# Performance work log

Hardware: AMD Instinct MI355X
Metric: run time of the kernel (lower is better)

The kernel has to match this reference:

```python
import jax, jax.numpy as jnp
import numpy as np

B, T, DIM, HEADS, DH, MLP = 2, 1024, 768, 8, 96, 3072
EPS = 1e-6


def _rms_norm(x, w):
    return x * jax.lax.rsqrt(jnp.mean(x * x, axis=-1, keepdims=True) + EPS) * w


def _rotate_half(x):
    x1, x2 = jnp.split(x, 2, axis=-1)
    return jnp.concatenate([-x2, x1], axis=-1)


def _l2norm(x):
    n = jnp.sqrt(jnp.sum(x * x, axis=-1, keepdims=True))
    return x / jnp.maximum(n, 1e-12)


def setup_inputs() -> dict:
    key = jax.random.key(0)
    ks = jax.random.split(key, 16)
    def rn(k, shape, s=0.02):
        return jax.random.normal(k, shape, jnp.float32) * s
    return {
        'x_stream1': jax.random.normal(ks[0], (B, T, DIM), jnp.float32),
        'x_stream2': jax.random.normal(ks[1], (B, T, DIM), jnp.float32),
        'p_emb': jax.random.normal(ks[2], (B, 1, 1024), jnp.float32),
        'mod_w1': rn(ks[3], (1024, 512)), 'mod_b1': jnp.zeros((512,), jnp.float32),
        'mod_w2': rn(ks[4], (512, DIM * 12)), 'mod_b2': jnp.zeros((DIM * 12,), jnp.float32),
        'norm11_w': jnp.ones((DIM,), jnp.float32), 'norm12_w': jnp.ones((DIM,), jnp.float32),
        'qkv_w': rn(ks[5], (DIM, 3 * DIM)), 'qkv_b': jnp.zeros((3 * DIM,), jnp.float32),
        'qkv2_w': rn(ks[6], (DIM, 3 * DIM)), 'qkv2_b': jnp.zeros((3 * DIM,), jnp.float32),
        'qk_scale': jnp.full((DH,), 10.0, jnp.float32),
        'out_w': rn(ks[7], (DIM, DIM)), 'out_b': jnp.zeros((DIM,), jnp.float32),
        'norm21_w': jnp.ones((DIM,), jnp.float32), 'norm22_w': jnp.ones((DIM,), jnp.float32),
        'mlp1_w1': rn(ks[8], (DIM, MLP)), 'mlp1_b1': jnp.zeros((MLP,), jnp.float32),
        'mlp1_w2': rn(ks[9], (MLP, DIM)), 'mlp1_b2': jnp.zeros((DIM,), jnp.float32),
        'mlp2_w1': rn(ks[10], (DIM, MLP)), 'mlp2_b1': jnp.zeros((MLP,), jnp.float32),
        'mlp2_w2': rn(ks[11], (MLP, DIM)), 'mlp2_b2': jnp.zeros((DIM,), jnp.float32),
    }


def _forward(x_stream1, x_stream2, p_emb, mod_w1, mod_b1, mod_w2, mod_b2,
             norm11_w, norm12_w, qkv_w, qkv_b, qkv2_w, qkv2_b, qk_scale,
             out_w, out_b, norm21_w, norm22_w,
             mlp1_w1, mlp1_b1, mlp1_w2, mlp1_b2,
             mlp2_w1, mlp2_b1, mlp2_w2, mlp2_b2):
    Bc, Tc, D = x_stream1.shape
    # modulation MLP: SiLU -> Linear -> SiLU -> Linear -> 12 chunks of [B, D]
    h = jax.nn.silu(p_emb[:, 0, :])
    h = jax.nn.silu(h @ mod_w1 + mod_b1)
    mod = h @ mod_w2 + mod_b2
    (m1s, m1h, m1g, m2s, m2h, m2g,
     m3s, m3h, m3g, m4s, m4h, m4g) = [m[:, None, :] for m in jnp.split(mod, 12, axis=1)]

    xm1 = _rms_norm(x_stream1, norm11_w) * (1 + m1s) + m1h
    xm2 = _rms_norm(x_stream2, norm12_w) * (1 + m2s) + m2h

    q1, k1, v1 = jnp.split(xm1 @ qkv_w + qkv_b, 3, axis=-1)
    q2, k2, v2 = jnp.split(xm2 @ qkv2_w + qkv2_b, 3, axis=-1)
    q = jnp.concatenate([q1, q2], axis=1)  # [B, 2T, D]
    k = jnp.concatenate([k1, k2], axis=1)
    v = jnp.concatenate([v1, v2], axis=1)
    N = 2 * Tc

    def to_heads(x):
        return x.reshape(Bc, N, HEADS, DH).transpose(0, 2, 1, 3)  # [B, H, N, dh]
    q, k, v = to_heads(q), to_heads(k), to_heads(v)

    # RoPE (inv_freq computed in bf16 as in the original, then used in fp32)
    inv_freq = (1.0 / (10000.0 ** (jnp.arange(0, DH, 2, dtype=jnp.float32) / DH))).astype(jnp.bfloat16).astype(jnp.float32)
    t = jnp.arange(N, dtype=jnp.float32)
    freqs = t[:, None] * inv_freq[None, :]
    emb = jnp.concatenate([freqs, freqs], axis=-1)  # [N, dh]
    cos, sin = jnp.cos(emb), jnp.sin(emb)
    q = q * cos + _rotate_half(q) * sin
    k = k * cos + _rotate_half(k) * sin

    # QK-Norm
    q = _l2norm(q) * qk_scale
    k = _l2norm(k) * qk_scale

    scores = jnp.einsum('bhid,bhjd->bhij', q, k) * (DH ** -0.5)
    probs = jax.nn.softmax(scores, axis=-1)
    attn = jnp.einsum('bhij,bhjd->bhid', probs, v)
    attn = attn.transpose(0, 2, 1, 3).reshape(Bc, N, D)
    attn = attn @ out_w + out_b

    x1 = x_stream1 + attn[:, :Tc, :] * m1g
    x2 = x_stream2 + attn[:, Tc:, :] * m2g

    xn1 = _rms_norm(x1, norm21_w) * (1 + m3s) + m3h
    mlp1 = jax.nn.gelu(xn1 @ mlp1_w1 + mlp1_b1, approximate=False) @ mlp1_w2 + mlp1_b2
    xn2 = _rms_norm(x2, norm22_w) * (1 + m4s) + m4h
    mlp2 = jax.nn.gelu(xn2 @ mlp2_w1 + mlp2_b1, approximate=False) @ mlp2_w2 + mlp2_b2

    return (x1 + mlp1 * m3g, x2 + mlp2 * m4g)


def reference(x_stream1, x_stream2, p_emb, mod_w1, mod_b1, mod_w2, mod_b2,
              norm11_w, norm12_w, qkv_w, qkv_b, qkv2_w, qkv2_b, qk_scale,
              out_w, out_b, norm21_w, norm22_w,
              mlp1_w1, mlp1_b1, mlp1_w2, mlp1_b2,
              mlp2_w1, mlp2_b1, mlp2_w2, mlp2_b2):
    return _forward(x_stream1, x_stream2, p_emb, mod_w1, mod_b1, mod_w2, mod_b2,
                    norm11_w, norm12_w, qkv_w, qkv_b, qkv2_w, qkv2_b, qk_scale,
                    out_w, out_b, norm21_w, norm22_w,
                    mlp1_w1, mlp1_b1, mlp1_w2, mlp1_b2,
                    mlp2_w1, mlp2_b1, mlp2_w2, mlp2_b2)
```

## Files before the change

kernel.cpp:

```cpp
#include <hip/hip_runtime.h>
#include <hip/hip_bf16.h>
#include <cstdint>
#include <math.h>

#define BB 2
#define TT 1024
#define DIMM 768
#define NHEADS 8
#define DHH 96
#define MLPD 3072
#define NN 2048

typedef unsigned short u16;
using short8 = __attribute__((ext_vector_type(8))) short;
using f32x4  = __attribute__((ext_vector_type(4))) float;
using f32x16 = __attribute__((ext_vector_type(16))) float;
using int4v  = __attribute__((ext_vector_type(4))) int;
union S8I4 { int4v i; short8 s; };

static constexpr float kEps = 1e-6f;

__device__ __forceinline__ float siluf(float x){ return x / (1.f + expf(-x)); }
__device__ __forceinline__ float geluf(float x){ return 0.5f*x*(1.f + erff(x*0.7071067811865475f)); }
__device__ __forceinline__ float bf16_rne(float x){
  uint32_t u = __float_as_uint(x);
  u = (u + 0x7fffu + ((u >> 16) & 1u)) & 0xffff0000u;
  return __uint_as_float(u);
}
__device__ __forceinline__ u16 f2b(float x){
  uint32_t u = __float_as_uint(x);
  return (u16)((u + 0x7fffu + ((u >> 16) & 1u)) >> 16);
}
__device__ __forceinline__ float b2f(u16 b){
  return __uint_as_float(((uint32_t)b) << 16);
}
__device__ __forceinline__ int cvtpk(float lo, float hi){
  int d; asm("v_cvt_pk_bf16_f32 %0, %1, %2" : "=v"(d) : "v"(lo), "v"(hi)); return d;
}
__device__ __forceinline__ void gload16(const void* g, void* l){
  __builtin_amdgcn_global_load_lds((const __attribute__((address_space(1))) unsigned int*)g,
                                   (__attribute__((address_space(3))) unsigned int*)l, 16, 0, 0);
}

__global__ __launch_bounds__(256) void mod_stage1_k(
    const float* __restrict__ p_emb, const float* __restrict__ w1,
    const float* __restrict__ b1, float* __restrict__ h2){
  __shared__ float sp[1024];
  const int b = blockIdx.x >> 1;
  const int obase = (blockIdx.x & 1) * 256;
  for (int i = threadIdx.x; i < 1024; i += 256)
    sp[i] = siluf(p_emb[b*1024 + i]);
  __syncthreads();
  const int o = obase + threadIdx.x;
  float acc = 0.f;
  for (int j = 0; j < 1024; ++j) acc += sp[j] * w1[j*512 + o];
  h2[b*512 + o] = siluf(acc + b1[o]);
}

__global__ __launch_bounds__(256) void mod_stage2_k(
    const float* __restrict__ h2, const float* __restrict__ w2,
    const float* __restrict__ b2, float* __restrict__ mod){
  __shared__ float sh[512];
  const int b = blockIdx.x / 36;
  const int obase = (blockIdx.x % 36) * 256;
  for (int i = threadIdx.x; i < 512; i += 256)
    sh[i] = h2[b*512 + i];
  __syncthreads();
  const int o = obase + threadIdx.x;
  float acc = 0.f;
  for (int j = 0; j < 512; ++j) acc += sh[j] * w2[j*9216 + o];
  mod[b*9216 + o] = acc + b2[o];
}

__global__ __launch_bounds__(256) void wt_all_k(
    const float* __restrict__ s0, u16* __restrict__ d0,
    const float* __restrict__ s1, u16* __restrict__ d1,
    const float* __restrict__ s2, u16* __restrict__ d2,
    const float* __restrict__ s3, u16* __restrict__ d3,
    const float* __restrict__ s4, u16* __restrict__ d4,
    const float* __restrict__ s5, u16* __restrict__ d5,
    const float* __restrict__ s6, u16* __restrict__ d6){
  const int bid = blockIdx.x;
  const float* S; u16* D; int K, N, lid;
  if      (bid < 432)  { S=s0; D=d0; K=768;  N=2304; lid=bid; }
  else if (bid < 864)  { S=s1; D=d1; K=768;  N=2304; lid=bid-432; }
  else if (bid < 1008) { S=s2; D=d2; K=768;  N=768;  lid=bid-864; }
  else if (bid < 1584) { S=s3; D=d3; K=768;  N=3072; lid=bid-1008; }
  else if (bid < 2160) { S=s4; D=d4; K=3072; N=768;  lid=bid-1584; }
  else if (bid < 2736) { S=s5; D=d5; K=768;  N=3072; lid=bid-2160; }
  else                 { S=s6; D=d6; K=3072; N=768;  lid=bid-2736; }
  const int nx = N >> 6;
  const int k0 = (lid / nx) * 64, n0 = (lid % nx) * 64;
  __shared__ float t[64][65];
  const int tx = threadIdx.x & 63, ty = threadIdx.x >> 6;
  for (int i = ty; i < 64; i += 4)
    t[i][tx] = S[(size_t)(k0+i)*N + n0 + tx];
  __syncthreads();
  for (int i = ty; i < 64; i += 4)
    D[(size_t)(n0+i)*K + k0 + tx] = f2b(t[tx][i]);
}

__global__ __launch_bounds__(256) void rmsnorm2_k(
    const float* __restrict__ x0, const float* __restrict__ w0, int cs0, int ch0, u16* __restrict__ o0,
    const float* __restrict__ x1, const float* __restrict__ w1, int cs1, int ch1, u16* __restrict__ o1,
    const float* __restrict__ mod){
  const int rowg = blockIdx.x;
  const int s = rowg >> 11;
  const int row = rowg & 2047;
  const float* x = s ? x1 : x0;
  const float* w = s ? w1 : w0;
  const int cs = s ? cs1 : cs0, ch = s ? ch1 : ch0;
  u16* out = s ? o1 : o0;
  const int b = row >> 10;
  const int tid = threadIdx.x;
  const float* xr = x + (size_t)row * DIMM;
  float v0 = xr[tid], v1 = xr[tid + 256], v2 = xr[tid + 512];
  float ss = v0*v0 + v1*v1 + v2*v2;
  __shared__ float red[4];
  for (int m = 1; m < 64; m <<= 1) ss += __shfl_xor(ss, m, 64);
  if ((tid & 63) == 0) red[tid >> 6] = ss;
  __syncthreads();
  float tot = red[0] + red[1] + red[2] + red[3];
  float rms = rsqrtf(tot * (1.f/768.f) + kEps);
  const float* ms = mod + (size_t)b*9216 + (size_t)cs*768;
  const float* mh = mod + (size_t)b*9216 + (size_t)ch*768;
  u16* orow = out + (size_t)row * DIMM;
  orow[tid]       = f2b(v0*rms*w[tid]      *(1.f+ms[tid])       + mh[tid]);
  orow[tid + 256] = f2b(v1*rms*w[tid+256]  *(1.f+ms[tid+256])   + mh[tid+256]);
  orow[tid + 512] = f2b(v2*rms*w[tid+512]  *(1.f+ms[tid+512])   + mh[tid+512]);
}

template<int EPI, int DUAL>
__global__ __launch_bounds__(256, 6) void gemm64_k(
    const u16* __restrict__ A0, const u16* __restrict__ Bt0,
    const float* __restrict__ bias0, void* __restrict__ C0,
    const u16* __restrict__ A1, const u16* __restrict__ Bt1,
    const float* __restrict__ bias1, void* __restrict__ C1,
    int M, int N, int K){
  __shared__ u16 As[2][64*32];
  __shared__ u16 Bs[2][64*32];
  const int z = DUAL ? blockIdx.z : 0;
  const u16* A      = z ? A1 : A0;
  const u16* Bt     = z ? Bt1 : Bt0;
  const float* bias = z ? bias1 : bias0;
  void* C           = z ? C1 : C0;
  const int tid = threadIdx.x;
  const int w = tid >> 6, l = tid & 63;
  const int wr = w >> 1, wc = w & 1;
  const int la = l & 15, hi4 = l >> 4;
  const int m0 = blockIdx.y*64, n0 = blockIdx.x*64;
  f32x4 acc[2][2] = {};
  const int nk = K >> 5;
  const int srow = tid >> 2;
  const int scol = ((tid & 3) ^ ((srow >> 1) & 3)) * 8;
  const u16* Ap = A  + (size_t)(m0 + srow)*K + scol;
  const u16* Bp = Bt + (size_t)(n0 + srow)*K + scol;
  #define STAGE(buf, kofs) { \
    gload16(Ap + (kofs), &As[buf][tid*8]); \
    gload16(Bp + (kofs), &Bs[buf][tid*8]); }
  STAGE(0, 0);
  __syncthreads();
  const int rslot = (hi4 ^ ((l >> 1) & 3)) * 8;
  for (int kt = 0; kt < nk; ++kt){
    const int cur = kt & 1;
    if (kt + 1 < nk) STAGE(cur^1, (kt+1) << 5);
    short8 af[2], bf[2];
    #pragma unroll
    for (int mi = 0; mi < 2; ++mi)
      af[mi] = *(const short8*)(&As[cur][(wr*32 + mi*16 + la)*32 + rslot]);
    #pragma unroll
    for (int ni = 0; ni < 2; ++ni)
      bf[ni] = *(const short8*)(&Bs[cur][(wc*32 + ni*16 + la)*32 + rslot]);
    #pragma unroll
    for (int mi = 0; mi < 2; ++mi)
      #pragma unroll
      for (int ni = 0; ni < 2; ++ni)
        acc[mi][ni] = __builtin_amdgcn_mfma_f32_16x16x32_bf16(af[mi], bf[ni], acc[mi][ni], 0, 0, 0);
    __syncthreads();
  }
  #undef STAGE
  #pragma unroll
  for (int mi = 0; mi < 2; ++mi){
    #pragma unroll
    for (int ni = 0; ni < 2; ++ni){
      const int n = n0 + wc*32 + ni*16 + la;
      const float bv = bias[n];
      #pragma unroll
      for (int rr = 0; rr < 4; ++rr){
        const int m = m0 + wr*32 + mi*16 + hi4*4 + rr;
        float v = acc[mi][ni][rr] + bv;
        if constexpr (EPI == 2) v = geluf(v);
        ((u16*)C)[(size_t)m*N + n] = f2b(v);
      }
    }
  }
}

template<int EPI, int DUAL>
__global__ __launch_bounds__(1024) void gemm16_k(
    const u16* __restrict__ A0, const u16* __restrict__ Bt0,
    const float* __restrict__ bias0,
    const u16* __restrict__ A1, const u16* __restrict__ Bt1,
    const float* __restrict__ bias1,
    const float* __restrict__ mod, const float* __restrict__ X0,
    const float* __restrict__ X1, float* __restrict__ O0,
    float* __restrict__ O1, int cg0, int cg1,
    int M, int N, int K){
  __shared__ char lds[131072];
  const int bid = blockIdx.x;
  const int xcd = bid & 7, kk = bid >> 3;
  const int g = xcd + 8*(kk/6);
  const int x = kk % 6;
  int by, z;
  if constexpr (DUAL){ by = g & 15; z = g >> 4; } else { by = g; z = 0; }
  const u16* A      = z ? A1 : A0;
  const u16* Bt     = z ? Bt1 : Bt0;
  const float* bias = z ? bias1 : bias0;
  const int tid = threadIdx.x;
  const int w = tid >> 6, l = tid & 63;
  const int kg = w >> 2, gw = w & 3;
  const int m0 = by*128, n0 = x*128;
  const int wr = gw >> 1, wc = gw & 1;
  const int la = l & 15, hi4 = l >> 4;
  u16* AsG = (u16*)(lds + kg*32768);
  u16* BsG = (u16*)(lds + kg*32768 + 16384);
  const int Kg = K >> 2;
  const int nk = Kg >> 5;
  const int kbase = kg * Kg;
  f32x4 acc[4][4] = {};
  #pragma unroll
  for (int it = 0; it < 2; ++it){
    const int sb = gw*128 + it*64;
    const int s = sb + l;
    const int row = s >> 2, scol = ((s & 3) ^ ((row >> 1) & 3)) * 8;
    gload16(A  + (size_t)(m0+row)*K + kbase + scol, AsG + sb*8);
    gload16(Bt + (size_t)(n0+row)*K + kbase + scol, BsG + sb*8);
  }
  __syncthreads();
  const int rslot = (hi4 ^ ((l >> 1) & 3)) * 8;
  for (int kt = 0; kt < nk; ++kt){
    const int cur = kt & 1;
    if (kt + 1 < nk){
      const int k0n = kbase + ((kt+1) << 5);
      #pragma unroll
      for (int it = 0; it < 2; ++it){
        const int sb = gw*128 + it*64;
        const int s = sb + l;
        const int row = s >> 2, scol = ((s & 3) ^ ((row >> 1) & 3)) * 8;
        gload16(A  + (size_t)(m0+row)*K + k0n + scol, AsG + (cur^1)*4096 + sb*8);
        gload16(Bt + (size_t)(n0+row)*K + k0n + scol, BsG + (cur^1)*4096 + sb*8);
      }
    }
    short8 af[4], bf[4];
    #pragma unroll
    for (int mi = 0; mi < 4; ++mi)
      af[mi] = *(const short8*)(AsG + cur*4096 + (wr*64 + mi*16 + la)*32 + rslot);
    #pragma unroll
    for (int ni = 0; ni < 4; ++ni)
      bf[ni] = *(const short8*)(BsG + cur*4096 + (wc*64 + ni*16 + la)*32 + rslot);
    #pragma unroll
    for (int mi = 0; mi < 4; ++mi)
      #pragma unroll
      for (int ni = 0; ni < 4; ++ni)
        acc[mi][ni] = __builtin_amdgcn_mfma_f32_16x16x32_bf16(af[mi], bf[ni], acc[mi][ni], 0, 0, 0);
    __syncthreads();
  }
  float* c0 = (float*)lds;
  float* c1 = (float*)(lds + 65536);
  #define WRACC(cb) { \
    _Pragma("unroll") for (int mi = 0; mi < 4; ++mi) \
    _Pragma("unroll") for (int ni = 0; ni < 4; ++ni) \
    _Pragma("unroll") for (int rr = 0; rr < 4; ++rr) \
      (cb)[(wr*64+mi*16+hi4*4+rr)*128 + wc*64+ni*16+la] = acc[mi][ni][rr]; }
  #define RDACC(cb) { \
    _Pragma("unroll") for (int mi = 0; mi < 4; ++mi) \
    _Pragma("unroll") for (int ni = 0; ni < 4; ++ni) \
    _Pragma("unroll") for (int rr = 0; rr < 4; ++rr) \
      acc[mi][ni][rr] += (cb)[(wr*64+mi*16+hi4*4+rr)*128 + wc*64+ni*16+la]; }
  if (kg == 1) WRACC(c0);
  if (kg == 3) WRACC(c1);
  __syncthreads();
  if (kg == 0) RDACC(c0);
  if (kg == 2) RDACC(c1);
  __syncthreads();
  if (kg == 2) WRACC(c0);
  __syncthreads();
  if (kg == 0){
    RDACC(c0);
    #pragma unroll
    for (int mi = 0; mi < 4; ++mi){
      #pragma unroll
      for (int ni = 0; ni < 4; ++ni){
        const int n = n0 + wc*64 + ni*16 + la;
        const float bv = bias[n];
        #pragma unroll
        for (int rr = 0; rr < 4; ++rr){
          const int m = m0 + wr*64 + mi*16 + hi4*4 + rr;
          float v = acc[mi][ni][rr] + bv;
          if constexpr (EPI == 3){
            const int bb = m >> 11, ss = (m >> 10) & 1, t = m & 1023;
            const float* X = ss ? X1 : X0;
            float* O = ss ? O1 : O0;
            const float gmod = mod[(size_t)bb*9216 + (size_t)(ss ? cg1 : cg0)*768 + n];
            const size_t oi = ((size_t)(bb*1024 + t))*768 + n;
            O[oi] = X[oi] + v*gmod;
          } else {
            float* O = z ? O1 : O0;
            const int cg = z ? cg1 : cg0;
            const int bb = m >> 10;
            const float gmod = mod[(size_t)bb*9216 + (size_t)cg*768 + n];
            O[(size_t)m*N + n] += v*gmod;
          }
        }
      }
    }
  }
  #undef WRACC
  #undef RDACC
}

__global__ __launch_bounds__(256) void build_qkv_k(
    const u16* __restrict__ qkv1, const u16* __restrict__ qkv2,
    const float* __restrict__ qk_scale,
    u16* __restrict__ Q, u16* __restrict__ K, u16* __restrict__ V){
  const int wid = threadIdx.x >> 6;
  const int lane = threadIdx.x & 63;
  const int row = blockIdx.x * 4 + wid;
  const int n = row & 2047;
  const int h = (row >> 11) & 7;
  const int b = row >> 14;
  const u16* src = (n < TT) ? (qkv1 + ((size_t)b*TT + n) * 2304)
                            : (qkv2 + ((size_t)b*TT + (n - TT)) * 2304);
  const int col = h * DHH;
  const bool act = lane < 48;
  float q0=0,q1=0,k0=0,k1=0,v0=0,v1=0,c=1.f,s=0.f,sc0=0,sc1=0;
  if (act){
    q0 = b2f(src[col + lane]);        q1 = b2f(src[col + lane + 48]);
    k0 = b2f(src[768 + col + lane]);  k1 = b2f(src[768 + col + lane + 48]);
    v0 = b2f(src[1536 + col + lane]); v1 = b2f(src[1536 + col + lane + 48]);
    float inv = bf16_rne((float)(1.0 / pow(10000.0, (2.0 * lane) / 96.0)));
    float ang = (float)n * inv;
    c = cosf(ang); s = sinf(ang);
    sc0 = qk_scale[lane]; sc1 = qk_scale[lane + 48];
  }
  float qr0 = q0*c - q1*s, qr1 = q1*c + q0*s;
  float kr0 = k0*c - k1*s, kr1 = k1*c + k0*s;
  float ssq = qr0*qr0 + qr1*qr1;
  float ssk = kr0*kr0 + kr1*kr1;
  for (int m = 1; m < 64; m <<= 1){ ssq += __shfl_xor(ssq, m, 64); ssk += __shfl_xor(ssk, m, 64); }
  float rq = 1.f / fmaxf(sqrtf(ssq), 1e-12f);
  float rk = 1.f / fmaxf(sqrtf(ssk), 1e-12f);
  const float sscale = 0.1020620726159658f;
  if (act){
    size_t base = (size_t)row * DHH;
    Q[base + lane]      = f2b(qr0*rq*sc0*sscale);  Q[base + lane + 48] = f2b(qr1*rq*sc1*sscale);
    K[base + lane]      = f2b(kr0*rk*sc0);         K[base + lane + 48] = f2b(kr1*rk*sc1);
    V[base + lane]      = f2b(v0);                 V[base + lane + 48] = f2b(v1);
  }
}

__global__ __launch_bounds__(256) void vtrans_k(
    const u16* __restrict__ Vtmp, u16* __restrict__ Vt){
  __shared__ u16 t[32][33];
  const int bh = blockIdx.z;
  const int n0 = blockIdx.x*32, d0 = blockIdx.y*32;
  const int tx = threadIdx.x & 31, ty = threadIdx.x >> 5;
  for (int i = ty; i < 32; i += 8)
    t[i][tx] = Vtmp[((size_t)bh*NN + n0+i)*DHH + d0 + tx];
  __syncthreads();
  for (int i = ty; i < 32; i += 8)
    Vt[((size_t)bh*DHH + d0+i)*NN + n0 + tx] = t[tx][i];
}

#define CROW(r) (((r)&3) + 8*((r)>>2) + 4*hi)
#define SMAXC 10.5f
#define BUILD_PA(dst, vec, basei) { \
  int a1_ = cvtpk(vec[basei+0], vec[basei+1]); \
  int b1_ = cvtpk(vec[basei+4], vec[basei+5]); \
  asm("v_permlane32_swap_b32 %0, %1" : "+v"(a1_), "+v"(b1_)); \
  int a2_ = cvtpk(vec[basei+2], vec[basei+3]); \
  int b2_ = cvtpk(vec[basei+6], vec[basei+7]); \
  asm("v_permlane32_swap_b32 %0, %1" : "+v"(a2_), "+v"(b2_)); \
  S8I4 u_; u_.i = (int4v){a1_, a2_, b1_, b2_}; dst = u_.s; }

__global__ __launch_bounds__(512) void attn_mfma_k(
    const u16* __restrict__ Qg, const u16* __restrict__ Kg,
    const u16* __restrict__ Vtg, u16* __restrict__ AO){
  __shared__ u16 Ks[2][2][64*128];
  __shared__ u16 Vs[2][2][96*64];
  const int bh = blockIdx.x >> 4;
  const int qblk = blockIdx.x & 15;
  const int b = bh >> 3, h = bh & 7;
  const int tid = threadIdx.x;
  const int w = tid >> 6, l = tid & 63;
  const int g2 = w >> 2, wq = w & 3;
  const int gtid = tid & 255;
  const int hi = l >> 5, li = l & 31;
  const int q0w = qblk*128 + wq*32;
  const int kvbase = g2 * 1024;

  short8 qf[6];
  {
    const u16* qrow = Qg + ((size_t)bh*NN + q0w + li)*DHH;
    #pragma unroll
    for (int ks = 0; ks < 6; ++ks)
      qf[ks] = *(const short8*)(qrow + ks*16 + hi*8);
  }

  f32x16 o0, o1, o2;
  #pragma unroll
  for (int r = 0; r < 16; ++r){ o0[r]=0.f; o1[r]=0.f; o2[r]=0.f; }
  float lrun = 0.f;

  {
    #pragma unroll
    for (int it = 0; it < 3; ++it){
      const int s = gtid + it*256;
      const int krow = s/12, ksl = s%12;
      short8 kv = *(const short8*)(Kg + ((size_t)bh*NN + kvbase + krow)*DHH + ksl*8);
      *(short8*)((char*)&Ks[g2][0][0] + krow*256 + ((ksl ^ (krow&7))<<4)) = kv;
      const int vrow = s >> 3, vsl = s & 7;
      short8 vv = *(const short8*)(Vtg + ((size_t)bh*DHH + vrow)*NN + kvbase + vsl*8);
      *(short8*)((char*)&Vs[g2][0][0] + vrow*128 + ((vsl ^ (vrow&7))<<4)) = vv;
    }
  }
  __syncthreads();

  const int NT2 = 16;
  for (int t = 0; t < NT2; ++t){
    const int cur = t & 1;
    short8 kst[3], vst[3];
    if (t + 1 < NT2){
      const int kv0 = kvbase + (t+1)*64;
      #pragma unroll
      for (int it = 0; it < 3; ++it){
        const int s = gtid + it*256;
        const int krow = s/12, ksl = s%12;
        kst[it] = *(const short8*)(Kg + ((size_t)bh*NN + kv0 + krow)*DHH + ksl*8);
        const int vrow = s >> 3, vsl = s & 7;
        vst[it] = *(const short8*)(Vtg + ((size_t)bh*DHH + vrow)*NN + kv0 + vsl*8);
      }
    }
    f32x16 s0, s1;
    #pragma unroll
    for (int r = 0; r < 16; ++r){ s0[r]=0.f; s1[r]=0.f; }
    #pragma unroll
    for (int ks = 0; ks < 6; ++ks){
      const int sl = ks*2 + hi;
      short8 kf0 = *(const short8*)((const char*)&Ks[g2][cur][0] + li*256      + ((sl ^ (li&7))<<4));
      short8 kf1 = *(const short8*)((const char*)&Ks[g2][cur][0] + (32+li)*256 + ((sl ^ ((32+li)&7))<<4));
      s0 = __builtin_amdgcn_mfma_f32_32x32x16_bf16(kf0, qf[ks], s0, 0, 0, 0);
      s1 = __builtin_amdgcn_mfma_f32_32x32x16_bf16(kf1, qf[ks], s1, 0, 0, 0);
    }
    float ps = 0.f;
    #pragma unroll
    for (int r = 0; r < 16; ++r){
      float pa = __expf(s0[r] - SMAXC);
      float pb = __expf(s1[r] - SMAXC);
      s0[r] = pa; s1[r] = pb; ps += pa + pb;
    }
    ps += __shfl_xor(ps, 32);
    lrun += ps;
    short8 pa0, pa1, pa2, pa3;
    BUILD_PA(pa0, s0, 0); BUILD_PA(pa1, s0, 8);
    BUILD_PA(pa2, s1, 0); BUILD_PA(pa3, s1, 8);
    #pragma unroll
    for (int dt = 0; dt < 3; ++dt){
      const int drow = dt*32 + li;
      const char* vb_base = (const char*)&Vs[g2][cur][0] + drow*128;
      f32x16* op = (dt==0)? &o0 : (dt==1)? &o1 : &o2;
      {
        short8 vb = *(const short8*)(vb_base + (((0*2+hi) ^ (drow&7))<<4));
        *op = __builtin_amdgcn_mfma_f32_32x32x16_bf16(pa0, vb, *op, 0, 0, 0);
      }
      {
        short8 vb = *(const short8*)(vb_base + (((1*2+hi) ^ (drow&7))<<4));
        *op = __builtin_amdgcn_mfma_f32_32x32x16_bf16(pa1, vb, *op, 0, 0, 0);
      }
      {
        short8 vb = *(const short8*)(vb_base + (((2*2+hi) ^ (drow&7))<<4));
        *op = __builtin_amdgcn_mfma_f32_32x32x16_bf16(pa2, vb, *op, 0, 0, 0);
      }
      {
        short8 vb = *(const short8*)(vb_base + (((3*2+hi) ^ (drow&7))<<4));
        *op = __builtin_amdgcn_mfma_f32_32x32x16_bf16(pa3, vb, *op, 0, 0, 0);
      }
    }
    __syncthreads();
    if (t + 1 < NT2){
      #pragma unroll
      for (int it = 0; it < 3; ++it){
        const int s = gtid + it*256;
        const int krow = s/12, ksl = s%12;
        *(short8*)((char*)&Ks[g2][cur^1][0] + krow*256 + ((ksl ^ (krow&7))<<4)) = kst[it];
        const int vrow = s >> 3, vsl = s & 7;
        *(short8*)((char*)&Vs[g2][cur^1][0] + vrow*128 + ((vsl ^ (vrow&7))<<4)) = vst[it];
      }
      __syncthreads();
    }
  }

  float* cmb = (float*)&Ks[0][0][0];
  float* cl  = (float*)&Vs[0][0][0];
  if (g2 == 1){
    #pragma unroll
    for (int r = 0; r < 16; ++r){
      cmb[((wq*16 + r)*3 + 0)*64 + l] = o0[r];
      cmb[((wq*16 + r)*3 + 1)*64 + l] = o1[r];
      cmb[((wq*16 + r)*3 + 2)*64 + l] = o2[r];
    }
    if (l < 32) cl[wq*32 + l] = lrun;
  }
  __syncthreads();
  if (g2 == 0){
    #pragma unroll
    for (int r = 0; r < 16; ++r){
      o0[r] += cmb[((wq*16 + r)*3 + 0)*64 + l];
      o1[r] += cmb[((wq*16 + r)*3 + 1)*64 + l];
      o2[r] += cmb[((wq*16 + r)*3 + 2)*64 + l];
    }
    lrun += cl[wq*32 + li];
    const float linv = 1.f / lrun;
    #pragma unroll
    for (int r = 0; r < 16; ++r){
      const float lr = __shfl(linv, CROW(r), 64);
      const int n = q0w + CROW(r);
      u16* dst = AO + ((size_t)b*NN + n)*DIMM + h*DHH + li;
      dst[0]  = f2b(o0[r]*lr);
      dst[32] = f2b(o1[r]*lr);
      dst[64] = f2b(o2[r]*lr);
    }
  }
}

static constexpr size_t W_QKV1T = 0;
static constexpr size_t W_QKV2T = W_QKV1T + 3538944;
static constexpr size_t W_OUTT  = W_QKV2T + 3538944;
static constexpr size_t W_M1W1T = W_OUTT  + 1179648;
static constexpr size_t W_M1W2T = W_M1W1T + 4718592;
static constexpr size_t W_M2W1T = W_M1W2T + 4718592;
static constexpr size_t W_M2W2T = W_M2W1T + 4718592;
static constexpr size_t O_MODH  = W_M2W2T + 4718592;
static constexpr size_t O_MODB  = O_MODH + 4096;
static constexpr size_t DYN     = O_MODB + 73728;
static constexpr size_t O_XM1   = DYN;
static constexpr size_t O_XM2   = O_XM1 + 3145728;
static constexpr size_t O_QKV1  = O_XM2 + 3145728;
static constexpr size_t O_QKV2  = O_QKV1 + 9437184;
static constexpr size_t O_QB    = O_QKV2 + 9437184;
static constexpr size_t O_KB    = O_QB + 6291456;
static constexpr size_t O_VTMP  = O_KB + 6291456;
static constexpr size_t O_PF    = O_VTMP + 6291456;
static constexpr size_t O_VT    = O_QKV1;
static constexpr size_t O_AO    = O_QKV2;
static constexpr size_t O_H1    = O_QB;
static constexpr size_t O_H2    = O_PF;

extern "C" void kernel_launch(void* const* d_in, const int* in_sizes, int n_in,
                              void* d_out, int out_size, void* d_ws, size_t ws_size,
                              hipStream_t stream){
  const float* x_s1   = (const float*)d_in[0];
  const float* x_s2   = (const float*)d_in[1];
  const float* p_emb  = (const float*)d_in[2];
  const float* mod_w1 = (const float*)d_in[3];
  const float* mod_b1 = (const float*)d_in[4];
  const float* mod_w2 = (const float*)d_in[5];
  const float* mod_b2 = (const float*)d_in[6];
  const float* n11_w  = (const float*)d_in[7];
  const float* n12_w  = (const float*)d_in[8];
  const float* qkv_w  = (const float*)d_in[9];
  const float* qkv_b  = (const float*)d_in[10];
  const float* qkv2_w = (const float*)d_in[11];
  const float* qkv2_b = (const float*)d_in[12];
  const float* qk_sc  = (const float*)d_in[13];
  const float* out_w  = (const float*)d_in[14];
  const float* out_b  = (const float*)d_in[15];
  const float* n21_w  = (const float*)d_in[16];
  const float* n22_w  = (const float*)d_in[17];
  const float* m1w1   = (const float*)d_in[18];
  const float* m1b1   = (const float*)d_in[19];
  const float* m1w2   = (const float*)d_in[20];
  const float* m1b2   = (const float*)d_in[21];
  const float* m2w1   = (const float*)d_in[22];
  const float* m2b1   = (const float*)d_in[23];
  const float* m2w2   = (const float*)d_in[24];
  const float* m2b2   = (const float*)d_in[25];

  char* ws = (char*)d_ws;
  u16* qkv1t = (u16*)(ws + W_QKV1T);
  u16* qkv2t = (u16*)(ws + W_QKV2T);
  u16* outt  = (u16*)(ws + W_OUTT);
  u16* w11t  = (u16*)(ws + W_M1W1T);
  u16* w12t  = (u16*)(ws + W_M1W2T);
  u16* w21t  = (u16*)(ws + W_M2W1T);
  u16* w22t  = (u16*)(ws + W_M2W2T);
  float* h2b  = (float*)(ws + O_MODH);
  float* modb = (float*)(ws + O_MODB);
  u16* xm1  = (u16*)(ws + O_XM1);
  u16* xm2  = (u16*)(ws + O_XM2);
  u16* qkv1 = (u16*)(ws + O_QKV1);
  u16* qkv2 = (u16*)(ws + O_QKV2);
  u16* Qb   = (u16*)(ws + O_QB);
  u16* Kb   = (u16*)(ws + O_KB);
  u16* Vtmp = (u16*)(ws + O_VTMP);
  u16* Vt   = (u16*)(ws + O_VT);
  u16* AO   = (u16*)(ws + O_AO);
  u16* H1   = (u16*)(ws + O_H1);
  u16* H2   = (u16*)(ws + O_H2);

  float* out0 = (float*)d_out;
  float* out1 = out0 + (size_t)BB*TT*DIMM;

  wt_all_k<<<3312, 256, 0, stream>>>(qkv_w, qkv1t, qkv2_w, qkv2t, out_w, outt,
                                     m1w1, w11t, m1w2, w12t, m2w1, w21t, m2w2, w22t);

  mod_stage1_k<<<4, 256, 0, stream>>>(p_emb, mod_w1, mod_b1, h2b);
  mod_stage2_k<<<72, 256, 0, stream>>>(h2b, mod_w2, mod_b2, modb);

  rmsnorm2_k<<<2*BB*TT, 256, 0, stream>>>(x_s1, n11_w, 0, 1, xm1,
                                          x_s2, n12_w, 3, 4, xm2, modb);

  gemm64_k<1,1><<<dim3(36, 32, 2), 256, 0, stream>>>(
      xm1, qkv1t, qkv_b, qkv1, xm2, qkv2t, qkv2_b, qkv2, 2048, 2304, 768);

  build_qkv_k<<<(BB*NHEADS*NN)/4, 256, 0, stream>>>(qkv1, qkv2, qk_sc, Qb, Kb, Vtmp);

  vtrans_k<<<dim3(NN/32, DHH/32, 16), 256, 0, stream>>>(Vtmp, Vt);

  attn_mfma_k<<<16*16, 512, 0, stream>>>(Qb, Kb, Vt, AO);

  gemm16_k<3,0><<<192, 1024, 0, stream>>>(
      AO, outt, out_b, AO, outt, out_b,
      modb, x_s1, x_s2, out0, out1, 2, 5, 4096, 768, 768);

  rmsnorm2_k<<<2*BB*TT, 256, 0, stream>>>(out0, n21_w, 6, 7, xm1,
                                          out1, n22_w, 9, 10, xm2, modb);

  gemm64_k<2,1><<<dim3(48, 32, 2), 256, 0, stream>>>(
      xm1, w11t, m1b1, H1, xm2, w21t, m2b1, H2, 2048, 3072, 768);

  gemm16_k<4,1><<<192, 1024, 0, stream>>>(
      H1, w12t, m1b2, H2, w22t, m2b2,
      modb, nullptr, nullptr, out0, out1, 8, 11, 2048, 768, 3072);
}
```

Before: 298.5 us.

## Simplify attention to single KV group, move out-proj to gemm64, shrink transpose tiles

Attention drops the two-group split-KV scheme (512 threads, double-buffered LDS, cross-group combine) in favour of 256 threads that each walk the full KV sequence with a single LDS buffer. The output projection moves from the 1024-thread split-K gemm16 kernel to the 64x64 gemm64 kernel, which gains a residual-gated epilogue. The weight transpose kernel switches from 64x64 to 32x32 tiles, launching four times as many blocks. Halving attention parallelism and removing double buffering risks exposing load latency, while the other changes alter grid shapes and occupancy.

```diff
diff --git a/kernel.cpp b/kernel.cpp
--- a/kernel.cpp
+++ b/kernel.cpp
@@ -82,21 +82,21 @@
     const float* __restrict__ s6, u16* __restrict__ d6){
   const int bid = blockIdx.x;
   const float* S; u16* D; int K, N, lid;
-  if      (bid < 432)  { S=s0; D=d0; K=768;  N=2304; lid=bid; }
-  else if (bid < 864)  { S=s1; D=d1; K=768;  N=2304; lid=bid-432; }
-  else if (bid < 1008) { S=s2; D=d2; K=768;  N=768;  lid=bid-864; }
-  else if (bid < 1584) { S=s3; D=d3; K=768;  N=3072; lid=bid-1008; }
-  else if (bid < 2160) { S=s4; D=d4; K=3072; N=768;  lid=bid-1584; }
-  else if (bid < 2736) { S=s5; D=d5; K=768;  N=3072; lid=bid-2160; }
-  else                 { S=s6; D=d6; K=3072; N=768;  lid=bid-2736; }
-  const int nx = N >> 6;
-  const int k0 = (lid / nx) * 64, n0 = (lid % nx) * 64;
-  __shared__ float t[64][65];
-  const int tx = threadIdx.x & 63, ty = threadIdx.x >> 6;
-  for (int i = ty; i < 64; i += 4)
+  if      (bid < 1728) { S=s0; D=d0; K=768;  N=2304; lid=bid; }
+  else if (bid < 3456) { S=s1; D=d1; K=768;  N=2304; lid=bid-1728; }
+  else if (bid < 4032) { S=s2; D=d2; K=768;  N=768;  lid=bid-3456; }
+  else if (bid < 6336) { S=s3; D=d3; K=768;  N=3072; lid=bid-4032; }
+  else if (bid < 8640) { S=s4; D=d4; K=3072; N=768;  lid=bid-6336; }
+  else if (bid < 10944){ S=s5; D=d5; K=768;  N=3072; lid=bid-8640; }
+  else                 { S=s6; D=d6; K=3072; N=768;  lid=bid-10944; }
+  const int nx = N >> 5;
+  const int k0 = (lid / nx) * 32, n0 = (lid % nx) * 32;
+  __shared__ float t[32][33];
+  const int tx = threadIdx.x & 31, ty = threadIdx.x >> 5;
+  for (int i = ty; i < 32; i += 8)
     t[i][tx] = S[(size_t)(k0+i)*N + n0 + tx];
   __syncthreads();
-  for (int i = ty; i < 64; i += 4)
+  for (int i = ty; i < 32; i += 8)
     D[(size_t)(n0+i)*K + k0 + tx] = f2b(t[tx][i]);
 }
 
@@ -136,6 +136,9 @@
     const float* __restrict__ bias0, void* __restrict__ C0,
     const u16* __restrict__ A1, const u16* __restrict__ Bt1,
     const float* __restrict__ bias1, void* __restrict__ C1,
+    const float* __restrict__ mod, const float* __restrict__ X0,
+    const float* __restrict__ X1, float* __restrict__ O0,
+    float* __restrict__ O1, int cg0, int cg1,
     int M, int N, int K){
   __shared__ u16 As[2][64*32];
   __shared__ u16 Bs[2][64*32];
@@ -190,7 +193,16 @@
         const int m = m0 + wr*32 + mi*16 + hi4*4 + rr;
         float v = acc[mi][ni][rr] + bv;
         if constexpr (EPI == 2) v = geluf(v);
-        ((u16*)C)[(size_t)m*N + n] = f2b(v);
+        if constexpr (EPI == 1 || EPI == 2){
+          ((u16*)C)[(size_t)m*N + n] = f2b(v);
+        } else {
+          const int bb = m >> 11, ss = (m >> 10) & 1, t = m & 1023;
+          const float* X = ss ? X1 : X0;
+          float* O = ss ? O1 : O0;
+          const float gmod = mod[(size_t)bb*9216 + (size_t)(ss ? cg1 : cg0)*768 + n];
+          const size_t oi = ((size_t)(bb*1024 + t))*768 + n;
+          O[oi] = X[oi] + v*gmod;
+        }
       }
     }
   }
@@ -202,8 +214,7 @@
     const float* __restrict__ bias0,
     const u16* __restrict__ A1, const u16* __restrict__ Bt1,
     const float* __restrict__ bias1,
-    const float* __restrict__ mod, const float* __restrict__ X0,
-    const float* __restrict__ X1, float* __restrict__ O0,
+    const float* __restrict__ mod, float* __restrict__ O0,
     float* __restrict__ O1, int cg0, int cg1,
     int M, int N, int K){
   __shared__ char lds[131072];
@@ -297,20 +308,11 @@
         for (int rr = 0; rr < 4; ++rr){
           const int m = m0 + wr*64 + mi*16 + hi4*4 + rr;
           float v = acc[mi][ni][rr] + bv;
-          if constexpr (EPI == 3){
-            const int bb = m >> 11, ss = (m >> 10) & 1, t = m & 1023;
-            const float* X = ss ? X1 : X0;
-            float* O = ss ? O1 : O0;
-            const float gmod = mod[(size_t)bb*9216 + (size_t)(ss ? cg1 : cg0)*768 + n];
-            const size_t oi = ((size_t)(bb*1024 + t))*768 + n;
-            O[oi] = X[oi] + v*gmod;
-          } else {
-            float* O = z ? O1 : O0;
-            const int cg = z ? cg1 : cg0;
-            const int bb = m >> 10;
-            const float gmod = mod[(size_t)bb*9216 + (size_t)cg*768 + n];
-            O[(size_t)m*N + n] += v*gmod;
-          }
+          float* O = z ? O1 : O0;
+          const int cg = z ? cg1 : cg0;
+          const int bb = m >> 10;
+          const float gmod = mod[(size_t)bb*9216 + (size_t)cg*768 + n];
+          O[(size_t)m*N + n] += v*gmod;
         }
       }
     }
@@ -383,21 +385,18 @@
   asm("v_permlane32_swap_b32 %0, %1" : "+v"(a2_), "+v"(b2_)); \
   S8I4 u_; u_.i = (int4v){a1_, a2_, b1_, b2_}; dst = u_.s; }
 
-__global__ __launch_bounds__(512) void attn_mfma_k(
+__global__ __launch_bounds__(256) void attn_mfma_k(
     const u16* __restrict__ Qg, const u16* __restrict__ Kg,
     const u16* __restrict__ Vtg, u16* __restrict__ AO){
-  __shared__ u16 Ks[2][2][64*128];
-  __shared__ u16 Vs[2][2][96*64];
+  __shared__ u16 Ks[64*128];
+  __shared__ u16 Vs[96*64];
   const int bh = blockIdx.x >> 4;
   const int qblk = blockIdx.x & 15;
   const int b = bh >> 3, h = bh & 7;
   const int tid = threadIdx.x;
   const int w = tid >> 6, l = tid & 63;
-  const int g2 = w >> 2, wq = w & 3;
-  const int gtid = tid & 255;
   const int hi = l >> 5, li = l & 31;
-  const int q0w = qblk*128 + wq*32;
-  const int kvbase = g2 * 1024;
+  const int q0w = qblk*128 + w*32;
 
   short8 qf[6];
   {
@@ -415,26 +414,25 @@
   {
     #pragma unroll
     for (int it = 0; it < 3; ++it){
-      const int s = gtid + it*256;
+      const int s = tid + it*256;
       const int krow = s/12, ksl = s%12;
-      short8 kv = *(const short8*)(Kg + ((size_t)bh*NN + kvbase + krow)*DHH + ksl*8);
-      *(short8*)((char*)&Ks[g2][0][0] + krow*256 + ((ksl ^ (krow&7))<<4)) = kv;
+      short8 kv = *(const short8*)(Kg + ((size_t)bh*NN + krow)*DHH + ksl*8);
+      *(short8*)((char*)Ks + krow*256 + ((ksl ^ (krow&7))<<4)) = kv;
       const int vrow = s >> 3, vsl = s & 7;
-      short8 vv = *(const short8*)(Vtg + ((size_t)bh*DHH + vrow)*NN + kvbase + vsl*8);
-      *(short8*)((char*)&Vs[g2][0][0] + vrow*128 + ((vsl ^ (vrow&7))<<4)) = vv;
-    }
-  }
-  __syncthreads();
-
-  const int NT2 = 16;
-  for (int t = 0; t < NT2; ++t){
-    const int cur = t & 1;
+      short8 vv = *(const short8*)(Vtg + ((size_t)bh*DHH + vrow)*NN + vsl*8);
+      *(short8*)((char*)Vs + vrow*128 + ((vsl ^ (vrow&7))<<4)) = vv;
+    }
+  }
+  __syncthreads();
+
+  const int NT = NN/64;
+  for (int t = 0; t < NT; ++t){
     short8 kst[3], vst[3];
-    if (t + 1 < NT2){
-      const int kv0 = kvbase + (t+1)*64;
+    if (t + 1 < NT){
+      const int kv0 = (t+1)*64;
       #pragma unroll
       for (int it = 0; it < 3; ++it){
-        const int s = gtid + it*256;
+        const int s = tid + it*256;
         const int krow = s/12, ksl = s%12;
         kst[it] = *(const short8*)(Kg + ((size_t)bh*NN + kv0 + krow)*DHH + ksl*8);
         const int vrow = s >> 3, vsl = s & 7;
@@ -447,8 +445,8 @@
     #pragma unroll
     for (int ks = 0; ks < 6; ++ks){
       const int sl = ks*2 + hi;
-      short8 kf0 = *(const short8*)((const char*)&Ks[g2][cur][0] + li*256      + ((sl ^ (li&7))<<4));
-      short8 kf1 = *(const short8*)((const char*)&Ks[g2][cur][0] + (32+li)*256 + ((sl ^ ((32+li)&7))<<4));
+      short8 kf0 = *(const short8*)((const char*)Ks + li*256      + ((sl ^ (li&7))<<4));
+      short8 kf1 = *(const short8*)((const char*)Ks + (32+li)*256 + ((sl ^ ((32+li)&7))<<4));
       s0 = __builtin_amdgcn_mfma_f32_32x32x16_bf16(kf0, qf[ks], s0, 0, 0, 0);
       s1 = __builtin_amdgcn_mfma_f32_32x32x16_bf16(kf1, qf[ks], s1, 0, 0, 0);
     }
@@ -467,7 +465,7 @@
     #pragma unroll
     for (int dt = 0; dt < 3; ++dt){
       const int drow = dt*32 + li;
-      const char* vb_base = (const char*)&Vs[g2][cur][0] + drow*128;
+      const char* vb_base = (const char*)Vs + drow*128;
       f32x16* op = (dt==0)? &o0 : (dt==1)? &o1 : &o2;
       {
         short8 vb = *(const short8*)(vb_base + (((0*2+hi) ^ (drow&7))<<4));
@@ -487,49 +485,28 @@
       }
     }
     __syncthreads();
-    if (t + 1 < NT2){
+    if (t + 1 < NT){
       #pragma unroll
       for (int it = 0; it < 3; ++it){
-        const int s = gtid + it*256;
+        const int s = tid + it*256;
         const int krow = s/12, ksl = s%12;
-        *(short8*)((char*)&Ks[g2][cur^1][0] + krow*256 + ((ksl ^ (krow&7))<<4)) = kst[it];
+        *(short8*)((char*)Ks + krow*256 + ((ksl ^ (krow&7))<<4)) = kst[it];
         const int vrow = s >> 3, vsl = s & 7;
-        *(short8*)((char*)&Vs[g2][cur^1][0] + vrow*128 + ((vsl ^ (vrow&7))<<4)) = vst[it];
+        *(short8*)((char*)Vs + vrow*128 + ((vsl ^ (vrow&7))<<4)) = vst[it];
       }
       __syncthreads();
     }
   }
 
-  float* cmb = (float*)&Ks[0][0][0];
-  float* cl  = (float*)&Vs[0][0][0];
-  if (g2 == 1){
-    #pragma unroll
-    for (int r = 0; r < 16; ++r){
-      cmb[((wq*16 + r)*3 + 0)*64 + l] = o0[r];
-      cmb[((wq*16 + r)*3 + 1)*64 + l] = o1[r];
-      cmb[((wq*16 + r)*3 + 2)*64 + l] = o2[r];
-    }
-    if (l < 32) cl[wq*32 + l] = lrun;
-  }
-  __syncthreads();
-  if (g2 == 0){
-    #pragma unroll
-    for (int r = 0; r < 16; ++r){
-      o0[r] += cmb[((wq*16 + r)*3 + 0)*64 + l];
-      o1[r] += cmb[((wq*16 + r)*3 + 1)*64 + l];
-      o2[r] += cmb[((wq*16 + r)*3 + 2)*64 + l];
-    }
-    lrun += cl[wq*32 + li];
-    const float linv = 1.f / lrun;
-    #pragma unroll
-    for (int r = 0; r < 16; ++r){
-      const float lr = __shfl(linv, CROW(r), 64);
-      const int n = q0w + CROW(r);
-      u16* dst = AO + ((size_t)b*NN + n)*DIMM + h*DHH + li;
-      dst[0]  = f2b(o0[r]*lr);
-      dst[32] = f2b(o1[r]*lr);
-      dst[64] = f2b(o2[r]*lr);
-    }
+  const float linv = 1.f / lrun;
+  #pragma unroll
+  for (int r = 0; r < 16; ++r){
+    const float lr = __shfl(linv, CROW(r), 64);
+    const int n = q0w + CROW(r);
+    u16* dst = AO + ((size_t)b*NN + n)*DIMM + h*DHH + li;
+    dst[0]  = f2b(o0[r]*lr);
+    dst[32] = f2b(o1[r]*lr);
+    dst[64] = f2b(o2[r]*lr);
   }
 }
 
@@ -611,8 +588,8 @@
   float* out0 = (float*)d_out;
   float* out1 = out0 + (size_t)BB*TT*DIMM;
 
-  wt_all_k<<<3312, 256, 0, stream>>>(qkv_w, qkv1t, qkv2_w, qkv2t, out_w, outt,
-                                     m1w1, w11t, m1w2, w12t, m2w1, w21t, m2w2, w22t);
+  wt_all_k<<<13248, 256, 0, stream>>>(qkv_w, qkv1t, qkv2_w, qkv2t, out_w, outt,
+                                      m1w1, w11t, m1w2, w12t, m2w1, w21t, m2w2, w22t);
 
   mod_stage1_k<<<4, 256, 0, stream>>>(p_emb, mod_w1, mod_b1, h2b);
   mod_stage2_k<<<72, 256, 0, stream>>>(h2b, mod_w2, mod_b2, modb);
@@ -621,25 +598,27 @@
                                           x_s2, n12_w, 3, 4, xm2, modb);
 
   gemm64_k<1,1><<<dim3(36, 32, 2), 256, 0, stream>>>(
-      xm1, qkv1t, qkv_b, qkv1, xm2, qkv2t, qkv2_b, qkv2, 2048, 2304, 768);
+      xm1, qkv1t, qkv_b, qkv1, xm2, qkv2t, qkv2_b, qkv2,
+      nullptr, nullptr, nullptr, nullptr, nullptr, 0, 0, 2048, 2304, 768);
 
   build_qkv_k<<<(BB*NHEADS*NN)/4, 256, 0, stream>>>(qkv1, qkv2, qk_sc, Qb, Kb, Vtmp);
 
   vtrans_k<<<dim3(NN/32, DHH/32, 16), 256, 0, stream>>>(Vtmp, Vt);
 
-  attn_mfma_k<<<16*16, 512, 0, stream>>>(Qb, Kb, Vt, AO);
-
-  gemm16_k<3,0><<<192, 1024, 0, stream>>>(
-      AO, outt, out_b, AO, outt, out_b,
+  attn_mfma_k<<<16*16, 256, 0, stream>>>(Qb, Kb, Vt, AO);
+
+  gemm64_k<3,0><<<dim3(12, 64, 1), 256, 0, stream>>>(
+      AO, outt, out_b, nullptr, AO, outt, out_b, nullptr,
       modb, x_s1, x_s2, out0, out1, 2, 5, 4096, 768, 768);
 
   rmsnorm2_k<<<2*BB*TT, 256, 0, stream>>>(out0, n21_w, 6, 7, xm1,
                                           out1, n22_w, 9, 10, xm2, modb);
 
   gemm64_k<2,1><<<dim3(48, 32, 2), 256, 0, stream>>>(
-      xm1, w11t, m1b1, H1, xm2, w21t, m2b1, H2, 2048, 3072, 768);
+      xm1, w11t, m1b1, H1, xm2, w21t, m2b1, H2,
+      nullptr, nullptr, nullptr, nullptr, nullptr, 0, 0, 2048, 3072, 768);
 
   gemm16_k<4,1><<<192, 1024, 0, stream>>>(
       H1, w12t, m1b2, H2, w22t, m2b2,
-      modb, nullptr, nullptr, out0, out1, 8, 11, 2048, 768, 3072);
-}
+      modb, out0, out1, 8, 11, 2048, 768, 3072);
+}
```

Result: slower. 309.7 us (+3.8%).
